# Kernel optimization log

Hardware: AMD Instinct MI355X
Metric: run time of the kernel (lower is better)

Reference implementation:

```python
import jax, jax.numpy as jnp
import numpy as np

R = 4        # in_transformations == out_transformations
FS = 3       # filter_size
PAD = 1
STRIDE = 1


def setup_inputs() -> dict:
    key = jax.random.key(0)
    k1, k2, k3 = jax.random.split(key, 3)
    B, Cin, O, K = 16, 64, 64, 4
    Ctot = Cin * R  # 256
    x = jax.random.normal(k1, (B, Ctot, 64, 64), dtype=jnp.float32)
    # kernel bank: [num_dynamic_kernels, out_channels, in_channels, f, f]
    kernel_bank = jax.random.normal(k2, (K, O, Cin, FS, FS), dtype=jnp.float32) * 0.05
    # routing fc: Linear(total_in_channels -> num_kernels)
    fc_w = jax.random.normal(k3, (K, Ctot), dtype=jnp.float32) * 0.05
    fc_b = jnp.zeros((K,), dtype=jnp.float32)
    return {"x": x, "kernel_bank": kernel_bank, "fc_w": fc_w, "fc_b": fc_b}


def reference(x, kernel_bank, fc_w, fc_b):
    B, Ctot, H, W = x.shape
    K, O, Cin, f, _ = kernel_bank.shape
    # --- dynamic routing: global avg pool -> fc -> sigmoid ---
    pooled = x.mean(axis=(2, 3))                                  # [B, Ctot]
    coeffs = jax.nn.sigmoid(pooled @ fc_w.T + fc_b)               # [B, K]
    # --- per-sample kernel synthesis ---
    base = jnp.einsum('bk,kocij->bocij', coeffs, kernel_bank)     # [B, O, Cin, f, f]
    # rotations rot90^k for k in 0..R-1 (matches torch.rot90 dims=(-2,-1))
    rotated = jnp.stack([jnp.rot90(base, k, axes=(-2, -1)) for k in range(R)], axis=1)  # [B, R, O, Cin, f, f]
    # block kernel: block (r_out, r_in) uses rotation index (r_out - r_in) % R,
    # so the r_in sum of convs becomes one conv over all R*Cin input channels.
    r_out = jnp.arange(R)[:, None]
    r_in = jnp.arange(R)[None, :]
    idx = (r_out - r_in) % R                                      # [R, R]
    big = rotated[:, idx]                                         # [B, R_out, R_in, O, Cin, f, f]
    big = big.transpose(0, 1, 3, 2, 4, 5, 6).reshape(B, R * O, R * Cin, f, f)
    # --- per-sample conv (vmapped over batch; each sample has its own kernel) ---
    def conv_one(xi, wi):
        return jax.lax.conv_general_dilated(
            xi[None], wi,
            window_strides=(STRIDE, STRIDE),
            padding=[(PAD, PAD), (PAD, PAD)],
            dimension_numbers=('NCHW', 'OIHW', 'NCHW'))[0]
    return jax.vmap(conv_one)(x, big)                             # [B, R*O, H, W]
```

## Files before the change

kernel.cpp:

```cpp
#include <hip/hip_runtime.h>
#include <hip/hip_bf16.h>
#include <math.h>

#define BATCH 16
#define CT    256
#define HW    64
#define OCH   64
#define NK    4
#define HP    66
#define NPIX  4356

typedef __attribute__((ext_vector_type(4)))  float  f32x4;
typedef __attribute__((ext_vector_type(8)))  short  s16x8;
typedef __attribute__((ext_vector_type(4)))  unsigned short u16x4;

#define GLOBAL_AS __attribute__((address_space(1)))
#define LDS_AS    __attribute__((address_space(3)))

__device__ __constant__ int c_rotsrc[4][9] = {
    {0,1,2,3,4,5,6,7,8},
    {2,5,8,1,4,7,0,3,6},
    {8,7,6,5,4,3,2,1,0},
    {6,3,0,7,4,1,8,5,2}
};

static __device__ inline unsigned short f2bf(float f) {
    union { __hip_bfloat16 h; unsigned short u; } cv;
    cv.h = __float2bfloat16(f);
    return cv.u;
}

__global__ __launch_bounds__(256) void xpose_pool(const float* __restrict__ x,
                                                  unsigned short* __restrict__ xTg,
                                                  float* __restrict__ partial) {
    const int ci0 = blockIdx.x * 64;
    const int g0  = ci0 >> 3;
    const int pr  = blockIdx.y;
    const int b   = blockIdx.z;
    const int t   = threadIdx.x;

    if (pr == 0 || pr == HP-1) {
        for (int u = t; u < 8*HP; u += 256) {
            int g = u / HP, c = u % HP;
            *(s16x8*)(xTg + ((((size_t)(b*32 + g0 + g))*NPIX) + pr*HP + c)*8) =
                (s16x8)(short)0;
        }
        return;
    }
    const int r = pr - 1;

    __shared__ unsigned short tile[64][70];
    const int cilH = t >> 4;
    const int c0   = (t & 15) * 4;
    #pragma unroll
    for (int i = 0; i < 4; ++i) {
        int cil = cilH + i*16;
        f32x4 v = *(const f32x4*)(x + (((size_t)(b*CT + ci0 + cil))*HW + r)*HW + c0);
        tile[cil][c0+0] = f2bf(v[0]);
        tile[cil][c0+1] = f2bf(v[1]);
        tile[cil][c0+2] = f2bf(v[2]);
        tile[cil][c0+3] = f2bf(v[3]);
        float s = v[0] + v[1] + v[2] + v[3];
        s += __shfl_xor(s, 1, 16);
        s += __shfl_xor(s, 2, 16);
        s += __shfl_xor(s, 4, 16);
        s += __shfl_xor(s, 8, 16);
        if ((t & 15) == 0)
            partial[((size_t)(b*HW) + r)*CT + ci0 + cil] = s;
    }
    __syncthreads();

    if (t < 16) {
        int g = t & 7, side = t >> 3;
        *(s16x8*)(xTg + ((((size_t)(b*32 + g0 + g))*NPIX) + pr*HP + side*(HP-1))*8) =
            (s16x8)(short)0;
    }
    #pragma unroll
    for (int i = 0; i < 4; ++i) {
        int u = i*256 + t;
        int c = u & 63, cil0 = (u >> 6) * 4;
        u16x4 w;
        w[0] = tile[cil0+0][c];
        w[1] = tile[cil0+1][c];
        w[2] = tile[cil0+2][c];
        w[3] = tile[cil0+3][c];
        *(u16x4*)(xTg + ((((size_t)(b*32 + g0 + (cil0>>3)))*NPIX) + pr*HP + c + 1)*8
                  + (cil0 & 4)) = w;
    }
}

__global__ __launch_bounds__(256) void coeff_kernel(const float* __restrict__ partial,
                                                    const float* __restrict__ fc_w,
                                                    const float* __restrict__ fc_b,
                                                    float* __restrict__ coeffs) {
    const int b = blockIdx.x;
    const int t = threadIdx.x;
    const float* pp = partial + (size_t)b*HW*CT + t;
    float s = 0.f;
    #pragma unroll 8
    for (int r = 0; r < HW; ++r) s += pp[(size_t)r*CT];
    __shared__ float pool[CT];
    pool[t] = s * (1.f / (HW*HW));
    __syncthreads();
    const int w = t >> 6, l = t & 63;
    float d = 0.f;
    for (int c = l; c < CT; c += 64) d += pool[c] * fc_w[w*CT + c];
    for (int off = 32; off; off >>= 1) d += __shfl_down(d, off, 64);
    if (l == 0)
        coeffs[b*NK + w] = 1.f / (1.f + expf(-(d + fc_b[w])));
}

__global__ __launch_bounds__(256) void bankrot_kernel(const float* __restrict__ bank,
                                                      float* __restrict__ P) {
    const int idx = blockIdx.x * 256 + threadIdx.x;
    const int o = idx & 63;
    const int c = (idx >> 6) & 63;
    const int k = idx >> 12;
    const float* bp = bank + ((size_t)((k*OCH + o)*64 + c))*9;
    float v[9];
    #pragma unroll
    for (int s = 0; s < 9; ++s) v[s] = bp[s];
    #pragma unroll
    for (int rr = 0; rr < 4; ++rr)
        #pragma unroll
        for (int s = 0; s < 9; ++s)
            P[(size_t)(((k*4 + rr)*9 + s))*4096 + c*64 + o] = v[c_rotsrc[rr][s]];
}

__global__ __launch_bounds__(256) void wbuild_kernel(const float* __restrict__ coeffs,
                                                     const float* __restrict__ P,
                                                     unsigned short* __restrict__ Wb) {
    const int cig = blockIdx.x;
    const int s   = blockIdx.y;
    const int co  = threadIdx.x;
    const int ro  = co >> 6;
    const int o   = co & 63;
    const int ri  = cig >> 3;
    const int rr  = (ro - ri) & 3;
    const int c8  = (cig & 7) * 8;

    float r[NK][8];
    #pragma unroll
    for (int k = 0; k < NK; ++k) {
        const float* pp = P + (size_t)(((k*4 + rr)*9 + s))*4096 + o;
        #pragma unroll
        for (int q = 0; q < 8; ++q)
            r[k][q] = pp[(c8 + q)*64];
    }
    #pragma unroll
    for (int b = 0; b < BATCH; ++b) {
        const float cf0 = coeffs[b*NK+0], cf1 = coeffs[b*NK+1];
        const float cf2 = coeffs[b*NK+2], cf3 = coeffs[b*NK+3];
        s16x8 w;
        #pragma unroll
        for (int q = 0; q < 8; ++q) {
            float v = cf0*r[0][q] + cf1*r[1][q] + cf2*r[2][q] + cf3*r[3][q];
            w[q] = (short)f2bf(v);
        }
        *(s16x8*)(Wb + ((((size_t)(b*9 + s)*32 + cig)*256 + co) << 3)) = w;
    }
}

#define SLAB_U  266
#define CHUNK_U 1064
#define BUF_U   1088
#define MF(A_, B_, C_) __builtin_amdgcn_mfma_f32_16x16x32_bf16(A_, B_, C_, 0, 0, 0)

__global__ __launch_bounds__(256, 3) void conv_mfma(
        const unsigned short* __restrict__ xTg,
        const unsigned short* __restrict__ Wb,
        float* __restrict__ out) {
    const int bid  = blockIdx.x;
    const int b    = (bid & 7)*2 + ((bid >> 3) & 1);
    const int rest = bid >> 4;
    const int coT  = rest & 1;
    const int r0   = (rest >> 1) * 2;

    const int t    = threadIdx.x;
    const int w    = t >> 6;
    const int lane = t & 63;
    const int lo16 = lane & 15;
    const int hi4  = lane >> 4;
    const int wco  = w & 1;
    const int wrow = w >> 1;

    __shared__ __align__(16) unsigned short Xs[2*BUF_U*8];

    f32x4 acc[4][4];
    #pragma unroll
    for (int f = 0; f < 4; ++f)
        #pragma unroll
        for (int p = 0; p < 4; ++p)
            acc[f][p] = (f32x4)0.f;

    const unsigned short* Wlane = Wb +
        (((size_t)(b*9*32) + hi4)*256 + coT*128 + wco*64 + lo16)*8;

#define LOADA(DST, CH, S)                                                       \
    do {                                                                        \
        const unsigned short* wp = Wlane + (size_t)((S)*32 + (CH)*4)*2048;      \
        _Pragma("unroll")                                                       \
        for (int f_ = 0; f_ < 4; ++f_)                                          \
            DST[f_] = *(const s16x8*)(wp + f_*128);                             \
    } while (0)

#define STAGE(CH, BUF)                                                          \
    do {                                                                        \
        _Pragma("unroll")                                                       \
        for (int it = 0; it < 5; ++it) {                                        \
            int ubase = it*256 + w*64;                                          \
            if (ubase < CHUNK_U) {                                              \
                int u  = ubase + lane;                                          \
                int us = u > (CHUNK_U-3) ? (CHUNK_U-3) : u;  \
                int q  = us / SLAB_U;                                           \
                int pl = us - q*SLAB_U;                                         \
                const unsigned short* src = xTg +                               \
                    (((size_t)(b*32 + (CH)*4 + q))*NPIX + r0*HP + pl)*8;        \
                __builtin_amdgcn_global_load_lds(                               \
                    (const GLOBAL_AS void*)src,                                 \
                    (LDS_AS void*)(Xs + (size_t)((BUF)*BUF_U + ubase)*8),       \
                    16, 0, 0);                                                  \
            }                                                                   \
        }                                                                       \
    } while (0)

    STAGE(0, 0);
    __syncthreads();

    for (int ch = 0; ch < 8; ++ch) {
        s16x8 A[9][4];
        LOADA(A[0], ch, 0);
        LOADA(A[1], ch, 1);
        __builtin_amdgcn_sched_barrier(0);
        if (ch < 7) STAGE(ch+1, (ch+1) & 1);

        const char* Xb = (const char*)Xs + (ch & 1)*(BUF_U*16)
                         + hi4*(SLAB_U*16) + lo16*16;

        #pragma unroll
        for (int s = 0; s < 9; ++s) {
            if (s < 7) LOADA(A[s+2], ch, s+2);
            const int dr = s/3, dc = s%3;
            const int rowoff = (wrow + dr)*HP + dc;
            s16x8 bf0 = *(const s16x8*)(Xb + (rowoff +  0)*16);
            s16x8 bf1 = *(const s16x8*)(Xb + (rowoff + 16)*16);
            s16x8 bf2 = *(const s16x8*)(Xb + (rowoff + 32)*16);
            s16x8 bf3 = *(const s16x8*)(Xb + (rowoff + 48)*16);
            acc[0][0] = MF(A[s][0], bf0, acc[0][0]);
            acc[1][0] = MF(A[s][1], bf0, acc[1][0]);
            acc[2][0] = MF(A[s][2], bf0, acc[2][0]);
            acc[3][0] = MF(A[s][3], bf0, acc[3][0]);
            acc[0][1] = MF(A[s][0], bf1, acc[0][1]);
            acc[1][1] = MF(A[s][1], bf1, acc[1][1]);
            acc[2][1] = MF(A[s][2], bf1, acc[2][1]);
            acc[3][1] = MF(A[s][3], bf1, acc[3][1]);
            acc[0][2] = MF(A[s][0], bf2, acc[0][2]);
            acc[1][2] = MF(A[s][1], bf2, acc[1][2]);
            acc[2][2] = MF(A[s][2], bf2, acc[2][2]);
            acc[3][2] = MF(A[s][3], bf2, acc[3][2]);
            acc[0][3] = MF(A[s][0], bf3, acc[0][3]);
            acc[1][3] = MF(A[s][1], bf3, acc[1][3]);
            acc[2][3] = MF(A[s][2], bf3, acc[2][3]);
            acc[3][3] = MF(A[s][3], bf3, acc[3][3]);
        }
        __syncthreads();
    }
#undef STAGE
#undef LOADA

    const int row = r0 + wrow;
    #pragma unroll
    for (int f = 0; f < 4; ++f)
        #pragma unroll
        for (int p = 0; p < 4; ++p) {
            const int colb = p*16 + lo16;
            #pragma unroll
            for (int j = 0; j < 4; ++j) {
                int co = coT*128 + wco*64 + f*16 + hi4*4 + j;
                out[(((size_t)(b*CT + co))*HW + row)*HW + colb] = acc[f][p][j];
            }
        }
}

extern "C" void kernel_launch(void* const* d_in, const int* in_sizes, int n_in,
                              void* d_out, int out_size, void* d_ws, size_t ws_size,
                              hipStream_t stream) {
    const float* x    = (const float*)d_in[0];
    const float* bank = (const float*)d_in[1];
    const float* fc_w = (const float*)d_in[2];
    const float* fc_b = (const float*)d_in[3];
    float* out = (float*)d_out;

    char* wsb = (char*)d_ws;
    float* partial = (float*)wsb;
    float* Prot    = (float*)wsb;
    float* coeffs  = (float*)(wsb + 2359296);
    unsigned short* Wb  = (unsigned short*)(wsb + 2360320);
    unsigned short* xTg = (unsigned short*)(wsb + 21234688);

    xpose_pool<<<dim3(4, HP, BATCH), 256, 0, stream>>>(x, xTg, partial);
    coeff_kernel<<<BATCH, 256, 0, stream>>>(partial, fc_w, fc_b, coeffs);
    bankrot_kernel<<<64, 256, 0, stream>>>(bank, Prot);
    wbuild_kernel<<<dim3(32, 9), 256, 0, stream>>>(coeffs, Prot, Wb);
    conv_mfma<<<1024, 256, 0, stream>>>(xTg, Wb, out);
}
```

Measured before the change: 111.0 us.

## Shrink conv tiles to one output row per block and drop LDS double buffering

The conv kernel now gives each block a single output row (128 threads, 2 waves split over output channels) instead of two rows over 4 waves, which doubles the grid to 2048 blocks. The staged input slab shrinks to three padded rows per channel group. The LDS double buffer with prefetch of the next chunk is replaced by a single buffer that is loaded synchronously between two barriers each iteration. This cuts LDS use and raises block count for occupancy, but loses the overlap of global loads with MFMA work and lowers row reuse of staged input and weights.

```diff
diff --git a/kernel.cpp b/kernel.cpp
--- a/kernel.cpp
+++ b/kernel.cpp
@@ -161,12 +161,11 @@
     }
 }
 
-#define SLAB_U  266
-#define CHUNK_U 1064
-#define BUF_U   1088
+#define SLAB_U  202
+#define CHUNK_U 808
 #define MF(A_, B_, C_) __builtin_amdgcn_mfma_f32_16x16x32_bf16(A_, B_, C_, 0, 0, 0)
 
-__global__ __launch_bounds__(256, 3) void conv_mfma(
+__global__ __launch_bounds__(128, 4) void conv_mfma(
         const unsigned short* __restrict__ xTg,
         const unsigned short* __restrict__ Wb,
         float* __restrict__ out) {
@@ -174,17 +173,15 @@
     const int b    = (bid & 7)*2 + ((bid >> 3) & 1);
     const int rest = bid >> 4;
     const int coT  = rest & 1;
-    const int r0   = (rest >> 1) * 2;
+    const int r0   = rest >> 1;
 
     const int t    = threadIdx.x;
     const int w    = t >> 6;
     const int lane = t & 63;
     const int lo16 = lane & 15;
     const int hi4  = lane >> 4;
-    const int wco  = w & 1;
-    const int wrow = w >> 1;
-
-    __shared__ __align__(16) unsigned short Xs[2*BUF_U*8];
+
+    __shared__ __align__(16) unsigned short Xs[CHUNK_U*8];
 
     f32x4 acc[4][4];
     #pragma unroll
@@ -194,7 +191,7 @@
             acc[f][p] = (f32x4)0.f;
 
     const unsigned short* Wlane = Wb +
-        (((size_t)(b*9*32) + hi4)*256 + coT*128 + wco*64 + lo16)*8;
+        (((size_t)(b*9*32) + hi4)*256 + coT*128 + w*64 + lo16)*8;
 
 #define LOADA(DST, CH, S)                                                       \
     do {                                                                        \
@@ -204,44 +201,40 @@
             DST[f_] = *(const s16x8*)(wp + f_*128);                             \
     } while (0)
 
-#define STAGE(CH, BUF)                                                          \
+#define STAGE(CH)                                                               \
     do {                                                                        \
         _Pragma("unroll")                                                       \
-        for (int it = 0; it < 5; ++it) {                                        \
-            int ubase = it*256 + w*64;                                          \
+        for (int it = 0; it < 7; ++it) {                                        \
+            int ubase = it*128 + w*64;                                          \
             if (ubase < CHUNK_U) {                                              \
                 int u  = ubase + lane;                                          \
-                int us = u > (CHUNK_U-3) ? (CHUNK_U-3) : u;  \
-                int q  = us / SLAB_U;                                           \
-                int pl = us - q*SLAB_U;                                         \
+                int q  = u / SLAB_U;                                            \
+                int pl = u - q*SLAB_U;                                          \
+                int plc = pl > 197 ? 197 : pl;         \
                 const unsigned short* src = xTg +                               \
-                    (((size_t)(b*32 + (CH)*4 + q))*NPIX + r0*HP + pl)*8;        \
+                    (((size_t)(b*32 + (CH)*4 + q))*NPIX + r0*HP + plc)*8;       \
                 __builtin_amdgcn_global_load_lds(                               \
                     (const GLOBAL_AS void*)src,                                 \
-                    (LDS_AS void*)(Xs + (size_t)((BUF)*BUF_U + ubase)*8),       \
+                    (LDS_AS void*)(Xs + (size_t)ubase * 8),                     \
                     16, 0, 0);                                                  \
             }                                                                   \
         }                                                                       \
     } while (0)
 
-    STAGE(0, 0);
-    __syncthreads();
-
     for (int ch = 0; ch < 8; ++ch) {
-        s16x8 A[9][4];
+        s16x8 A[10][4];
         LOADA(A[0], ch, 0);
-        LOADA(A[1], ch, 1);
-        __builtin_amdgcn_sched_barrier(0);
-        if (ch < 7) STAGE(ch+1, (ch+1) & 1);
-
-        const char* Xb = (const char*)Xs + (ch & 1)*(BUF_U*16)
-                         + hi4*(SLAB_U*16) + lo16*16;
+        __syncthreads();
+        STAGE(ch);
+        __syncthreads();
+
+        const char* Xb = (const char*)Xs + hi4*(SLAB_U*16) + lo16*16;
 
         #pragma unroll
         for (int s = 0; s < 9; ++s) {
-            if (s < 7) LOADA(A[s+2], ch, s+2);
+            if (s < 8) LOADA(A[s+1], ch, s+1);
             const int dr = s/3, dc = s%3;
-            const int rowoff = (wrow + dr)*HP + dc;
+            const int rowoff = dr*HP + dc;
             s16x8 bf0 = *(const s16x8*)(Xb + (rowoff +  0)*16);
             s16x8 bf1 = *(const s16x8*)(Xb + (rowoff + 16)*16);
             s16x8 bf2 = *(const s16x8*)(Xb + (rowoff + 32)*16);
@@ -263,12 +256,10 @@
             acc[2][3] = MF(A[s][2], bf3, acc[2][3]);
             acc[3][3] = MF(A[s][3], bf3, acc[3][3]);
         }
-        __syncthreads();
     }
 #undef STAGE
 #undef LOADA
 
-    const int row = r0 + wrow;
     #pragma unroll
     for (int f = 0; f < 4; ++f)
         #pragma unroll
@@ -276,8 +267,8 @@
             const int colb = p*16 + lo16;
             #pragma unroll
             for (int j = 0; j < 4; ++j) {
-                int co = coT*128 + wco*64 + f*16 + hi4*4 + j;
-                out[(((size_t)(b*CT + co))*HW + row)*HW + colb] = acc[f][p][j];
+                int co = coT*128 + w*64 + f*16 + hi4*4 + j;
+                out[(((size_t)(b*CT + co))*HW + r0)*HW + colb] = acc[f][p][j];
             }
         }
 }
@@ -302,5 +293,5 @@
     coeff_kernel<<<BATCH, 256, 0, stream>>>(partial, fc_w, fc_b, coeffs);
     bankrot_kernel<<<64, 256, 0, stream>>>(bank, Prot);
     wbuild_kernel<<<dim3(32, 9), 256, 0, stream>>>(coeffs, Prot, Wb);
-    conv_mfma<<<1024, 256, 0, stream>>>(xTg, Wb, out);
-}
+    conv_mfma<<<2048, 128, 0, stream>>>(xTg, Wb, out);
+}
```

Result: no change. 109.8 us (-1.1%).
